# Kernel optimization log

Hardware: AMD Instinct MI355X
Metric: run time of the kernel (lower is better)

The kernel has to match this reference:

```python
import jax, jax.numpy as jnp
import numpy as np

EMBED_DIM = 512
NUM_HEADS = 8
HEAD_DIM = EMBED_DIM // NUM_HEADS
SCALE = 1.0 / HEAD_DIM ** 0.5


def setup_inputs() -> dict:
    key = jax.random.key(0)
    ks = jax.random.split(key, 7)
    B, C, H, W = 8, EMBED_DIM, 32, 32
    x = jax.random.normal(ks[0], (B, C, H, W), dtype=jnp.float32)
    s = 1.0 / np.sqrt(EMBED_DIM)
    return {
        "x": x,
        "ln_gamma": jnp.ones((EMBED_DIM,), jnp.float32),
        "ln_beta": jnp.zeros((EMBED_DIM,), jnp.float32),
        "w_qkv": jax.random.uniform(ks[1], (EMBED_DIM, 3 * EMBED_DIM), jnp.float32, -s, s),
        "b_qkv": jax.random.uniform(ks[2], (3 * EMBED_DIM,), jnp.float32, -s, s),
        "w_proj": jax.random.uniform(ks[3], (EMBED_DIM, EMBED_DIM), jnp.float32, -s, s),
        "b_proj": jax.random.uniform(ks[4], (EMBED_DIM,), jnp.float32, -s, s),
    }


def reference(x, ln_gamma, ln_beta, w_qkv, b_qkv, w_proj, b_proj):
    B, C, H, W = x.shape
    N = H * W
    # LayerNorm over channel dim (applied in NHWC layout in the original)
    xs = x.reshape(B, C, N).transpose(0, 2, 1)  # [B, N, C]
    mu = jnp.mean(xs, axis=-1, keepdims=True)
    var = jnp.mean(jnp.square(xs - mu), axis=-1, keepdims=True)
    xn = (xs - mu) / jnp.sqrt(var + 1e-5) * ln_gamma + ln_beta
    # QKV projection
    qkv = xn @ w_qkv + b_qkv                        # [B, N, 3C]
    qkv = qkv.reshape(B, N, 3, NUM_HEADS, HEAD_DIM)
    q = qkv[:, :, 0].transpose(0, 2, 1, 3)         # [B, h, N, d]
    k = qkv[:, :, 1].transpose(0, 2, 1, 3)
    v = qkv[:, :, 2].transpose(0, 2, 1, 3)
    # Scaled dot-product attention (full N x N scores, as in source)
    attn = jnp.einsum('bhnd,bhmd->bhnm', q, k) * SCALE
    attn = jax.nn.softmax(attn, axis=-1)
    o = jnp.einsum('bhnm,bhmd->bhnd', attn, v)     # [B, h, N, d]
    o = o.transpose(0, 2, 1, 3).reshape(B, N, C)
    # Output projection (dropout is identity in eval)
    o = o @ w_proj + b_proj
    return o.transpose(0, 2, 1).reshape(B, C, H, W)
```

## Files before the change

kernel.cpp:

```cpp
#include <hip/hip_runtime.h>
#include <hip/hip_bf16.h>
#include <math.h>

#define B_   8
#define C_   512
#define NH_  8
#define HD_  64
#define NSP  1024
#define M_   (B_*NSP)
#define NQKV 1536
#define SCALE_ 0.125f
#define S2L_  0.18033688f

typedef __attribute__((ext_vector_type(8))) __bf16 bf16x8;
typedef __attribute__((ext_vector_type(4))) float  f32x4;

__device__ __forceinline__ unsigned short f2bf(float f) {
  unsigned int u = __float_as_uint(f);
  u = u + 0x7fffu + ((u >> 16) & 1u);
  return (unsigned short)(u >> 16);
}

__device__ __forceinline__ unsigned int pk2bf(float a, float b) {
  __hip_bfloat162 t = __float22bfloat162_rn(make_float2(a, b));
  unsigned int u; __builtin_memcpy(&u, &t, 4);
  return u;
}

__device__ __forceinline__ void async16(const unsigned short* g, unsigned short* l) {
  __builtin_amdgcn_global_load_lds(
      (const __attribute__((address_space(1))) void*)g,
      (__attribute__((address_space(3))) void*)l, 16, 0, 0);
}

__global__ void ln_stats_kernel(const float* __restrict__ x,
                                float* __restrict__ psum,
                                float* __restrict__ psum2) {
  int tx = threadIdx.x & 31, ty = threadIdx.x >> 5;
  int cg  = blockIdx.x & 3;
  int nch = (blockIdx.x >> 2) & 31;
  int b   = blockIdx.x >> 7;
  int n0 = nch * 32;
  const float* xp = x + (size_t)b * C_ * NSP + n0 + tx;
  float s = 0.f, s2 = 0.f;
  for (int c = cg * 128 + ty; c < cg * 128 + 128; c += 8) {
    float v = xp[(size_t)c * NSP];
    s += v; s2 += v * v;
  }
  __shared__ float sh_s[8][32], sh_s2[8][32];
  sh_s[ty][tx] = s; sh_s2[ty][tx] = s2;
  __syncthreads();
  if (ty == 0) {
    float S = 0.f, S2 = 0.f;
    for (int j = 0; j < 8; j++) { S += sh_s[j][tx]; S2 += sh_s2[j][tx]; }
    psum [cg * M_ + b * NSP + n0 + tx] = S;
    psum2[cg * M_ + b * NSP + n0 + tx] = S2;
  }
}

__global__ __launch_bounds__(256) void applyw_kernel(
    const float* __restrict__ x, const float* __restrict__ psum,
    const float* __restrict__ psum2, const float* __restrict__ gamma,
    const float* __restrict__ beta, const float* __restrict__ wqkv,
    const float* __restrict__ wproj, unsigned short* __restrict__ xn,
    unsigned short* __restrict__ wqkvT, unsigned short* __restrict__ wprojT) {
  int tid = threadIdx.x;
  __shared__ float tile[64][65];
  int tx = tid & 63, ty = tid >> 6;
  if (blockIdx.x >= 1024) {
    const float* W; unsigned short* WT; int NW, t;
    if (blockIdx.x < 1216) { W = wqkv;  WT = wqkvT;  NW = NQKV; t = blockIdx.x - 1024; }
    else                   { W = wproj; WT = wprojT; NW = C_;   t = blockIdx.x - 1216; }
    int ntiles = NW >> 6;
    int kt = t / ntiles, nt = t - kt * ntiles;
    for (int i = ty; i < 64; i += 4)
      tile[i][tx] = W[(size_t)(kt * 64 + i) * NW + nt * 64 + tx];
    __syncthreads();
    for (int i = ty; i < 64; i += 4)
      WT[(size_t)(nt * 64 + i) * C_ + kt * 64 + tx] = f2bf(tile[tx][i]);
    return;
  }
  __shared__ float smu[64], srs[64];
  int c0 = (blockIdx.x & 7) * 64;
  int n0 = ((blockIdx.x >> 3) & 15) * 64;
  int b  = blockIdx.x >> 7;
  if (tid < 64) {
    int n = b * NSP + n0 + tid;
    float s  = psum [n] + psum [M_ + n] + psum [2 * M_ + n] + psum [3 * M_ + n];
    float s2 = psum2[n] + psum2[M_ + n] + psum2[2 * M_ + n] + psum2[3 * M_ + n];
    float mu = s * (1.0f / C_);
    float var = s2 * (1.0f / C_) - mu * mu;
    smu[tid] = mu;
    srs[tid] = rsqrtf(var + 1e-5f);
  }
  const float* xp = x + ((size_t)b * C_ + c0) * NSP + n0;
  for (int i = ty; i < 64; i += 4)
    tile[i][tx] = xp[(size_t)i * NSP + tx];
  __syncthreads();
  float g = gamma[c0 + tx], be = beta[c0 + tx];
  unsigned short* op = xn + ((size_t)(b * NSP + n0)) * C_ + c0 + tx;
  for (int i = ty; i < 64; i += 4) {
    float v = (tile[tx][i] - smu[i]) * srs[i] * g + be;
    op[(size_t)i * C_] = f2bf(v);
  }
}

__global__ __launch_bounds__(256) void gemm_qkv_kernel(
    const unsigned short* __restrict__ A,
    const unsigned short* __restrict__ Bt,
    const float* __restrict__ bias,
    unsigned short* __restrict__ out0, unsigned short* __restrict__ out1) {
  __shared__ __align__(16) char smem[24576];
  int tid = threadIdx.x;
  int wave = tid >> 6, lane = tid & 63, quad = lane >> 4, l15 = lane & 15;
  int n0 = blockIdx.x * 128, m0 = blockIdx.y * 64;
  int wm = (wave >> 1) * 32, wn = (wave & 1) * 64;
  int srow = lane >> 2, schunk = (lane & 3) * 8;
  auto stage = [&](int k0, int buf) {
    unsigned short* As = (unsigned short*)(smem + buf * 12288);
    unsigned short* Bs = (unsigned short*)(smem + buf * 12288 + 4096);
    async16(A + (size_t)(m0 + wave * 16 + srow) * 512 + k0 + schunk,
            As + wave * 16 * 32 + lane * 8);
#pragma unroll
    for (int j = 0; j < 2; j++) {
      int r0 = (wave + 4 * j) * 16;
      async16(Bt + (size_t)(n0 + r0 + srow) * 512 + k0 + schunk, Bs + r0 * 32 + lane * 8);
    }
  };
  f32x4 acc[2][4] = {};
  stage(0, 0);
  for (int kt = 0; kt < 16; kt++) {
    int cur = kt & 1;
    __syncthreads();
    if (kt < 15) stage((kt + 1) * 32, cur ^ 1);
    unsigned short* As = (unsigned short*)(smem + cur * 12288);
    unsigned short* Bs = (unsigned short*)(smem + cur * 12288 + 4096);
    bf16x8 a[2], bb[4];
#pragma unroll
    for (int mt = 0; mt < 2; mt++)
      a[mt] = *(const bf16x8*)(As + (wm + mt * 16 + l15) * 32 + quad * 8);
#pragma unroll
    for (int nt = 0; nt < 4; nt++)
      bb[nt] = *(const bf16x8*)(Bs + (wn + nt * 16 + l15) * 32 + quad * 8);
#pragma unroll
    for (int mt = 0; mt < 2; mt++)
#pragma unroll
      for (int nt = 0; nt < 4; nt++)
        acc[mt][nt] = __builtin_amdgcn_mfma_f32_16x16x32_bf16(
            a[mt], bb[nt], acc[mt][nt], 0, 0, 0);
  }
  if (n0 < 1024) {
    float sc = ((n0 + wn) < 512) ? S2L_ : 1.0f;
#pragma unroll
    for (int mt = 0; mt < 2; mt++)
#pragma unroll
      for (int nt = 0; nt < 4; nt++)
#pragma unroll
        for (int r = 0; r < 4; r++) {
          int row = m0 + wm + mt * 16 + quad * 4 + r;
          int col = n0 + wn + nt * 16 + l15;
          out0[(size_t)row * 1024 + col] = f2bf((acc[mt][nt][r] + bias[col]) * sc);
        }
  } else {
    __syncthreads();
    unsigned short* buf = (unsigned short*)smem + wave * (32 * 17);
    int b = m0 >> 10, nbase = m0 & 1023;
    for (int nc = 0; nc < 4; nc++) {
#pragma unroll
      for (int mt = 0; mt < 2; mt++)
#pragma unroll
        for (int r = 0; r < 4; r++) {
          int col = n0 + wn + nc * 16 + l15;
          buf[(mt * 16 + quad * 4 + r) * 17 + l15] = f2bf(acc[mt][nc][r] + bias[col]);
        }
      int ml = lane & 31;
#pragma unroll
      for (int j = 0; j < 8; j++) {
        int cl = j * 2 + (lane >> 5);
        int crel = n0 - 1024 + wn + nc * 16 + cl;
        out1[((size_t)b * C_ + crel) * NSP + nbase + wm + ml] = buf[ml * 17 + cl];
      }
    }
  }
}

__global__ __launch_bounds__(256) void gemm_proj_kernel(
    const unsigned short* __restrict__ A,
    const unsigned short* __restrict__ Bt,
    const float* __restrict__ bias,
    float* __restrict__ O) {
  __shared__ __align__(16) char smem[20480];
  int tid = threadIdx.x;
  int wave = tid >> 6, lane = tid & 63, quad = lane >> 4, l15 = lane & 15;
  int n0 = blockIdx.x * 128, m0 = blockIdx.y * 32;
  int wm = (wave >> 1) * 16, wn = (wave & 1) * 64;
  int srow = lane >> 2, schunk = (lane & 3) * 8;
  auto stage = [&](int k0, int buf) {
    unsigned short* As = (unsigned short*)(smem + buf * 10240);
    unsigned short* Bs = (unsigned short*)(smem + buf * 10240 + 2048);
    if (wave < 2)
      async16(A + (size_t)(m0 + wave * 16 + srow) * 512 + k0 + schunk,
              As + wave * 16 * 32 + lane * 8);
#pragma unroll
    for (int j = 0; j < 2; j++) {
      int r0 = (wave + 4 * j) * 16;
      async16(Bt + (size_t)(n0 + r0 + srow) * 512 + k0 + schunk, Bs + r0 * 32 + lane * 8);
    }
  };
  f32x4 acc[4] = {};
  stage(0, 0);
  for (int kt = 0; kt < 16; kt++) {
    int cur = kt & 1;
    __syncthreads();
    if (kt < 15) stage((kt + 1) * 32, cur ^ 1);
    unsigned short* As = (unsigned short*)(smem + cur * 10240);
    unsigned short* Bs = (unsigned short*)(smem + cur * 10240 + 2048);
    bf16x8 a, bb[4];
    a = *(const bf16x8*)(As + (wm + l15) * 32 + quad * 8);
#pragma unroll
    for (int nt = 0; nt < 4; nt++)
      bb[nt] = *(const bf16x8*)(Bs + (wn + nt * 16 + l15) * 32 + quad * 8);
#pragma unroll
    for (int nt = 0; nt < 4; nt++)
      acc[nt] = __builtin_amdgcn_mfma_f32_16x16x32_bf16(a, bb[nt], acc[nt], 0, 0, 0);
  }
  __syncthreads();
  float* buf = (float*)smem + wave * (16 * 17);
  int b = m0 >> 10, nbase = m0 & 1023;
  int ml = lane & 15, cg = lane >> 4;
  for (int nc = 0; nc < 4; nc++) {
#pragma unroll
    for (int r = 0; r < 4; r++) {
      int col = n0 + wn + nc * 16 + l15;
      buf[(quad * 4 + r) * 17 + l15] = acc[nc][r] + bias[col];
    }
#pragma unroll
    for (int j = 0; j < 4; j++) {
      int cl = j * 4 + cg;
      int c = n0 + wn + nc * 16 + cl;
      O[((size_t)b * C_ + c) * NSP + nbase + wm + ml] = buf[ml * 17 + cl];
    }
  }
}

__global__ __launch_bounds__(256, 3) void attn_kernel(
    const unsigned short* __restrict__ qk,
    const unsigned short* __restrict__ vt,
    unsigned short* __restrict__ o_ws) {
  __shared__ __align__(16) unsigned short Ks[2][2][32][64];
  __shared__ __align__(16) unsigned short Vts[2][2][64][32];
  __shared__ __align__(16) unsigned short Ps[4][32][36];
  __shared__ __align__(16) float Cb[2][16][68];
  __shared__ float Lb[2][16];
  int tid = threadIdx.x;
  int wave = tid >> 6, lane = tid & 63, quad = lane >> 4, l15 = lane & 15;
  int qw = wave & 1, kh = wave >> 1;
  int b = blockIdx.x >> 3, h = blockIdx.x & 7;
  int q0 = blockIdx.y * 64 + qw * 32;
  int srow = lane >> 3, scc = lane & 7, swzK = scc ^ srow;
  int srow4 = lane >> 2, scc4 = lane & 3, swzV = scc4 ^ ((srow4 >> 1) & 3);
  uint4 ones4 = (l15 == 0) ? make_uint4(0x3F803F80u, 0x3F803F80u, 0x3F803F80u, 0x3F803F80u)
                           : make_uint4(0u, 0u, 0u, 0u);
  bf16x8 av5; __builtin_memcpy(&av5, &ones4, 16);
  bf16x8 bq[2][2];
#pragma unroll
  for (int mt = 0; mt < 2; mt++)
#pragma unroll
    for (int ks = 0; ks < 2; ks++)
      bq[mt][ks] = *(const bf16x8*)(
          qk + (size_t)(b * NSP + q0 + mt * 16 + l15) * 1024 +
          h * 64 + ks * 32 + quad * 8);
  auto stage = [&](int it, int buf) {
    int k0 = kh * 512 + it * 32;
#pragma unroll
    for (int g = 0; g < 2; g++) {
      int krow = qw * 16 + g * 8;
      async16(qk + (size_t)(b * NSP + k0 + krow + srow) * 1024 + 512 + h * 64 + swzK * 8,
              &Ks[buf][kh][krow][0]);
      int vrow = qw * 32 + g * 16;
      async16(vt + ((size_t)(b * C_ + h * 64 + vrow + srow4)) * NSP + k0 + swzV * 8,
              &Vts[buf][kh][vrow][0]);
    }
  };
  f32x4 ot[4][2] = {};
  f32x4 lacc[2] = {};
  stage(0, 0);
  for (int it = 0; it < 16; it++) {
    int cur = it & 1;
    __syncthreads();
    if (it < 15) stage(it + 1, cur ^ 1);
    bf16x8 ak[2][2];
#pragma unroll
    for (int n4 = 0; n4 < 2; n4++)
#pragma unroll
      for (int ks = 0; ks < 2; ks++)
        ak[n4][ks] = *(const bf16x8*)(
            &Ks[cur][kh][n4 * 16 + l15][((ks * 4 + quad) ^ (l15 & 7)) * 8]);
    f32x4 s[2][2] = {};
#pragma unroll
    for (int n4 = 0; n4 < 2; n4++)
#pragma unroll
      for (int mt = 0; mt < 2; mt++)
#pragma unroll
        for (int ks = 0; ks < 2; ks++)
          s[n4][mt] = __builtin_amdgcn_mfma_f32_16x16x32_bf16(
              ak[n4][ks], bq[mt][ks], s[n4][mt], 0, 0, 0);
#pragma unroll
    for (int mt = 0; mt < 2; mt++)
#pragma unroll
      for (int n4 = 0; n4 < 2; n4++) {
        float p0 = __builtin_amdgcn_exp2f(s[n4][mt][0]);
        float p1 = __builtin_amdgcn_exp2f(s[n4][mt][1]);
        float p2 = __builtin_amdgcn_exp2f(s[n4][mt][2]);
        float p3 = __builtin_amdgcn_exp2f(s[n4][mt][3]);
        *(uint2*)(&Ps[wave][mt * 16 + l15][n4 * 16 + quad * 4]) =
            make_uint2(pk2bf(p0, p1), pk2bf(p2, p3));
      }
    bf16x8 av[4], bp[2];
#pragma unroll
    for (int dt = 0; dt < 4; dt++)
      av[dt] = *(const bf16x8*)(
          &Vts[cur][kh][dt * 16 + l15][(quad ^ ((l15 >> 1) & 3)) * 8]);
#pragma unroll
    for (int mt = 0; mt < 2; mt++)
      bp[mt] = *(const bf16x8*)(&Ps[wave][mt * 16 + l15][quad * 8]);
#pragma unroll
    for (int dt = 0; dt < 4; dt++)
#pragma unroll
      for (int mt = 0; mt < 2; mt++)
        ot[dt][mt] = __builtin_amdgcn_mfma_f32_16x16x32_bf16(
            av[dt], bp[mt], ot[dt][mt], 0, 0, 0);
#pragma unroll
    for (int mt = 0; mt < 2; mt++)
      lacc[mt] = __builtin_amdgcn_mfma_f32_16x16x32_bf16(
          av5, bp[mt], lacc[mt], 0, 0, 0);
  }
#pragma unroll
  for (int mt = 0; mt < 2; mt++) {
    __syncthreads();
    if (kh == 1) {
#pragma unroll
      for (int dt = 0; dt < 4; dt++)
        *(f32x4*)&Cb[qw][l15][dt * 16 + quad * 4] = ot[dt][mt];
      if (quad == 0) Lb[qw][l15] = lacc[mt][0];
    }
    __syncthreads();
    if (kh == 0) {
#pragma unroll
      for (int dt = 0; dt < 4; dt++)
        ot[dt][mt] += *(const f32x4*)&Cb[qw][l15][dt * 16 + quad * 4];
      float lsum = lacc[mt][0] + Lb[qw][l15];
      float lv = __shfl(lsum, l15);
      float inv = 1.f / lv;
      size_t rowoff = (size_t)(b * NSP + q0 + mt * 16 + l15) * 512 + h * 64;
#pragma unroll
      for (int dt = 0; dt < 4; dt++)
        *(uint2*)(o_ws + rowoff + dt * 16 + quad * 4) =
            make_uint2(pk2bf(ot[dt][mt][0] * inv, ot[dt][mt][1] * inv),
                       pk2bf(ot[dt][mt][2] * inv, ot[dt][mt][3] * inv));
    }
  }
}

extern "C" void kernel_launch(void* const* d_in, const int* in_sizes, int n_in,
                              void* d_out, int out_size, void* d_ws, size_t ws_size,
                              hipStream_t stream) {
  const float* x     = (const float*)d_in[0];
  const float* gamma = (const float*)d_in[1];
  const float* beta  = (const float*)d_in[2];
  const float* wqkv  = (const float*)d_in[3];
  const float* bqkv  = (const float*)d_in[4];
  const float* wproj = (const float*)d_in[5];
  const float* bproj = (const float*)d_in[6];
  char* ws = (char*)d_ws;
  float*          psum   = (float*)ws;
  float*          psum2  = (float*)(ws + 131072);
  unsigned short* wqkvT  = (unsigned short*)(ws + 262144);
  unsigned short* wprojT = (unsigned short*)(ws + 1835008);
  unsigned short* qk_bf  = (unsigned short*)(ws + 2359296);
  unsigned short* vt_bf  = (unsigned short*)(ws + 19136512);
  unsigned short* xn_bf  = (unsigned short*)(ws + 27525120);
  unsigned short* o_bf   = xn_bf;
  float* out = (float*)d_out;

  ln_stats_kernel<<<1024, 256, 0, stream>>>(x, psum, psum2);
  applyw_kernel<<<1024 + 192 + 64, 256, 0, stream>>>(x, psum, psum2, gamma, beta,
                                                     wqkv, wproj, xn_bf, wqkvT, wprojT);
  gemm_qkv_kernel<<<dim3(NQKV / 128, M_ / 64), 256, 0, stream>>>(
      xn_bf, wqkvT, bqkv, qk_bf, vt_bf);
  attn_kernel<<<dim3(B_ * NH_, NSP / 64), 256, 0, stream>>>(qk_bf, vt_bf, o_bf);
  gemm_proj_kernel<<<dim3(C_ / 128, M_ / 32), 256, 0, stream>>>(
      o_bf, wprojT, bproj, out);
}
```

Measured before the change: 162.7 us.

## Rewrite attention with 32x32x16 MFMA, register-resident P and no split-K reduction

The attention kernel now uses 32x32x16 bf16 MFMAs, with each wave owning 32 query rows across the full key range. This removes the two-way key split and its LDS reduction. The probabilities are repacked in registers using v_permlane32_swap instead of going through an LDS P buffer, and the row sum is accumulated with scalar adds instead of an extra MFMA against a ones vector. Each block covers 128 queries with 64-key tiles, which halves the grid and lowers the occupancy target to 2 blocks, trading parallelism for fewer LDS round trips and less sync.

```diff
diff --git a/kernel.cpp b/kernel.cpp
--- a/kernel.cpp
+++ b/kernel.cpp
@@ -14,6 +14,7 @@
 
 typedef __attribute__((ext_vector_type(8))) __bf16 bf16x8;
 typedef __attribute__((ext_vector_type(4))) float  f32x4;
+typedef __attribute__((ext_vector_type(16))) float f32x16;
 
 __device__ __forceinline__ unsigned short f2bf(float f) {
   unsigned int u = __float_as_uint(f);
@@ -243,122 +244,97 @@
   }
 }
 
-__global__ __launch_bounds__(256, 3) void attn_kernel(
+__global__ __launch_bounds__(256, 2) void attn_kernel(
     const unsigned short* __restrict__ qk,
     const unsigned short* __restrict__ vt,
     unsigned short* __restrict__ o_ws) {
-  __shared__ __align__(16) unsigned short Ks[2][2][32][64];
-  __shared__ __align__(16) unsigned short Vts[2][2][64][32];
-  __shared__ __align__(16) unsigned short Ps[4][32][36];
-  __shared__ __align__(16) float Cb[2][16][68];
-  __shared__ float Lb[2][16];
+  __shared__ __align__(16) unsigned short Ks[2][64][64];
+  __shared__ __align__(16) unsigned short Vts[2][64][64];
   int tid = threadIdx.x;
-  int wave = tid >> 6, lane = tid & 63, quad = lane >> 4, l15 = lane & 15;
-  int qw = wave & 1, kh = wave >> 1;
+  int wave = tid >> 6, lane = tid & 63;
+  int l31 = lane & 31, hi = lane >> 5;
   int b = blockIdx.x >> 3, h = blockIdx.x & 7;
-  int q0 = blockIdx.y * 64 + qw * 32;
-  int srow = lane >> 3, scc = lane & 7, swzK = scc ^ srow;
-  int srow4 = lane >> 2, scc4 = lane & 3, swzV = scc4 ^ ((srow4 >> 1) & 3);
-  uint4 ones4 = (l15 == 0) ? make_uint4(0x3F803F80u, 0x3F803F80u, 0x3F803F80u, 0x3F803F80u)
-                           : make_uint4(0u, 0u, 0u, 0u);
-  bf16x8 av5; __builtin_memcpy(&av5, &ones4, 16);
-  bf16x8 bq[2][2];
-#pragma unroll
-  for (int mt = 0; mt < 2; mt++)
-#pragma unroll
-    for (int ks = 0; ks < 2; ks++)
-      bq[mt][ks] = *(const bf16x8*)(
-          qk + (size_t)(b * NSP + q0 + mt * 16 + l15) * 1024 +
-          h * 64 + ks * 32 + quad * 8);
+  int qb = blockIdx.y * 128 + wave * 32;
+  int sc8 = lane & 7, sr8 = lane >> 3;
+  int swz = sc8 ^ sr8;
+  bf16x8 bq[4];
+#pragma unroll
+  for (int ks = 0; ks < 4; ks++)
+    bq[ks] = *(const bf16x8*)(
+        qk + (size_t)(b * NSP + qb + l31) * 1024 + h * 64 + ks * 16 + hi * 8);
   auto stage = [&](int it, int buf) {
-    int k0 = kh * 512 + it * 32;
+    int k0 = it * 64;
 #pragma unroll
     for (int g = 0; g < 2; g++) {
-      int krow = qw * 16 + g * 8;
-      async16(qk + (size_t)(b * NSP + k0 + krow + srow) * 1024 + 512 + h * 64 + swzK * 8,
-              &Ks[buf][kh][krow][0]);
-      int vrow = qw * 32 + g * 16;
-      async16(vt + ((size_t)(b * C_ + h * 64 + vrow + srow4)) * NSP + k0 + swzV * 8,
-              &Vts[buf][kh][vrow][0]);
+      int row = wave * 16 + g * 8 + sr8;
+      async16(qk + (size_t)(b * NSP + k0 + row) * 1024 + 512 + h * 64 + swz * 8,
+              &Ks[buf][wave * 16 + g * 8][0]);
+      async16(vt + ((size_t)(b * C_ + h * 64 + row)) * NSP + k0 + swz * 8,
+              &Vts[buf][wave * 16 + g * 8][0]);
     }
   };
-  f32x4 ot[4][2] = {};
-  f32x4 lacc[2] = {};
+  f32x16 ot0 = {}, ot1 = {};
+  float lsum = 0.f;
   stage(0, 0);
   for (int it = 0; it < 16; it++) {
     int cur = it & 1;
     __syncthreads();
     if (it < 15) stage(it + 1, cur ^ 1);
-    bf16x8 ak[2][2];
-#pragma unroll
-    for (int n4 = 0; n4 < 2; n4++)
-#pragma unroll
-      for (int ks = 0; ks < 2; ks++)
-        ak[n4][ks] = *(const bf16x8*)(
-            &Ks[cur][kh][n4 * 16 + l15][((ks * 4 + quad) ^ (l15 & 7)) * 8]);
-    f32x4 s[2][2] = {};
-#pragma unroll
-    for (int n4 = 0; n4 < 2; n4++)
-#pragma unroll
-      for (int mt = 0; mt < 2; mt++)
-#pragma unroll
-        for (int ks = 0; ks < 2; ks++)
-          s[n4][mt] = __builtin_amdgcn_mfma_f32_16x16x32_bf16(
-              ak[n4][ks], bq[mt][ks], s[n4][mt], 0, 0, 0);
-#pragma unroll
-    for (int mt = 0; mt < 2; mt++)
-#pragma unroll
-      for (int n4 = 0; n4 < 2; n4++) {
-        float p0 = __builtin_amdgcn_exp2f(s[n4][mt][0]);
-        float p1 = __builtin_amdgcn_exp2f(s[n4][mt][1]);
-        float p2 = __builtin_amdgcn_exp2f(s[n4][mt][2]);
-        float p3 = __builtin_amdgcn_exp2f(s[n4][mt][3]);
-        *(uint2*)(&Ps[wave][mt * 16 + l15][n4 * 16 + quad * 4]) =
-            make_uint2(pk2bf(p0, p1), pk2bf(p2, p3));
+    bf16x8 bp[4];
+#pragma unroll
+    for (int kt = 0; kt < 2; kt++) {
+      f32x16 s = {};
+#pragma unroll
+      for (int ks = 0; ks < 4; ks++) {
+        bf16x8 ak = *(const bf16x8*)(
+            &Ks[cur][kt * 32 + l31][((ks * 2 + hi) ^ (l31 & 7)) * 8]);
+        s = __builtin_amdgcn_mfma_f32_32x32x16_bf16(ak, bq[ks], s, 0, 0, 0);
       }
-    bf16x8 av[4], bp[2];
-#pragma unroll
-    for (int dt = 0; dt < 4; dt++)
-      av[dt] = *(const bf16x8*)(
-          &Vts[cur][kh][dt * 16 + l15][(quad ^ ((l15 >> 1) & 3)) * 8]);
-#pragma unroll
-    for (int mt = 0; mt < 2; mt++)
-      bp[mt] = *(const bf16x8*)(&Ps[wave][mt * 16 + l15][quad * 8]);
-#pragma unroll
-    for (int dt = 0; dt < 4; dt++)
-#pragma unroll
-      for (int mt = 0; mt < 2; mt++)
-        ot[dt][mt] = __builtin_amdgcn_mfma_f32_16x16x32_bf16(
-            av[dt], bp[mt], ot[dt][mt], 0, 0, 0);
-#pragma unroll
-    for (int mt = 0; mt < 2; mt++)
-      lacc[mt] = __builtin_amdgcn_mfma_f32_16x16x32_bf16(
-          av5, bp[mt], lacc[mt], 0, 0, 0);
-  }
-#pragma unroll
-  for (int mt = 0; mt < 2; mt++) {
-    __syncthreads();
-    if (kh == 1) {
-#pragma unroll
-      for (int dt = 0; dt < 4; dt++)
-        *(f32x4*)&Cb[qw][l15][dt * 16 + quad * 4] = ot[dt][mt];
-      if (quad == 0) Lb[qw][l15] = lacc[mt][0];
-    }
-    __syncthreads();
-    if (kh == 0) {
-#pragma unroll
-      for (int dt = 0; dt < 4; dt++)
-        ot[dt][mt] += *(const f32x4*)&Cb[qw][l15][dt * 16 + quad * 4];
-      float lsum = lacc[mt][0] + Lb[qw][l15];
-      float lv = __shfl(lsum, l15);
-      float inv = 1.f / lv;
-      size_t rowoff = (size_t)(b * NSP + q0 + mt * 16 + l15) * 512 + h * 64;
-#pragma unroll
-      for (int dt = 0; dt < 4; dt++)
-        *(uint2*)(o_ws + rowoff + dt * 16 + quad * 4) =
-            make_uint2(pk2bf(ot[dt][mt][0] * inv, ot[dt][mt][1] * inv),
-                       pk2bf(ot[dt][mt][2] * inv, ot[dt][mt][3] * inv));
-    }
+      float p0 = __builtin_amdgcn_exp2f(s[0]),  p1 = __builtin_amdgcn_exp2f(s[1]);
+      float p2 = __builtin_amdgcn_exp2f(s[2]),  p3 = __builtin_amdgcn_exp2f(s[3]);
+      float p4 = __builtin_amdgcn_exp2f(s[4]),  p5 = __builtin_amdgcn_exp2f(s[5]);
+      float p6 = __builtin_amdgcn_exp2f(s[6]),  p7 = __builtin_amdgcn_exp2f(s[7]);
+      float p8 = __builtin_amdgcn_exp2f(s[8]),  p9 = __builtin_amdgcn_exp2f(s[9]);
+      float pa = __builtin_amdgcn_exp2f(s[10]), pb = __builtin_amdgcn_exp2f(s[11]);
+      float pc = __builtin_amdgcn_exp2f(s[12]), pd = __builtin_amdgcn_exp2f(s[13]);
+      float pe = __builtin_amdgcn_exp2f(s[14]), pf = __builtin_amdgcn_exp2f(s[15]);
+      lsum += ((p0 + p1) + (p2 + p3)) + ((p4 + p5) + (p6 + p7)) +
+              (((p8 + p9) + (pa + pb)) + ((pc + pd) + (pe + pf)));
+      unsigned int d0 = pk2bf(p0, p1), d1 = pk2bf(p2, p3);
+      unsigned int d2 = pk2bf(p4, p5), d3 = pk2bf(p6, p7);
+      unsigned int d4 = pk2bf(p8, p9), d5 = pk2bf(pa, pb);
+      unsigned int d6 = pk2bf(pc, pd), d7 = pk2bf(pe, pf);
+      asm volatile("v_permlane32_swap_b32 %0, %1" : "+v"(d0), "+v"(d2));
+      asm volatile("v_permlane32_swap_b32 %0, %1" : "+v"(d1), "+v"(d3));
+      asm volatile("v_permlane32_swap_b32 %0, %1" : "+v"(d4), "+v"(d6));
+      asm volatile("v_permlane32_swap_b32 %0, %1" : "+v"(d5), "+v"(d7));
+      uint4 f0 = make_uint4(d0, d1, d2, d3);
+      uint4 f1 = make_uint4(d4, d5, d6, d7);
+      __builtin_memcpy(&bp[kt * 2 + 0], &f0, 16);
+      __builtin_memcpy(&bp[kt * 2 + 1], &f1, 16);
+    }
+#pragma unroll
+    for (int kc = 0; kc < 4; kc++) {
+      bf16x8 av0 = *(const bf16x8*)(
+          &Vts[cur][l31][((kc * 2 + hi) ^ (l31 & 7)) * 8]);
+      ot0 = __builtin_amdgcn_mfma_f32_32x32x16_bf16(av0, bp[kc], ot0, 0, 0, 0);
+      bf16x8 av1 = *(const bf16x8*)(
+          &Vts[cur][32 + l31][(((kc * 2 + hi) ^ (l31 & 7)) ^ 0) * 8]);
+      ot1 = __builtin_amdgcn_mfma_f32_32x32x16_bf16(av1, bp[kc], ot1, 0, 0, 0);
+    }
+  }
+  float lv = __shfl(lsum, l31) + __shfl(lsum, l31 + 32);
+  float inv = 1.f / lv;
+  unsigned short* orow = o_ws + (size_t)(b * NSP + qb + l31) * 512 + h * 64;
+#pragma unroll
+  for (int g = 0; g < 4; g++) {
+    int d0 = 8 * g + 4 * hi;
+    *(uint2*)(orow + d0) =
+        make_uint2(pk2bf(ot0[4 * g + 0] * inv, ot0[4 * g + 1] * inv),
+                   pk2bf(ot0[4 * g + 2] * inv, ot0[4 * g + 3] * inv));
+    *(uint2*)(orow + 32 + d0) =
+        make_uint2(pk2bf(ot1[4 * g + 0] * inv, ot1[4 * g + 1] * inv),
+                   pk2bf(ot1[4 * g + 2] * inv, ot1[4 * g + 3] * inv));
   }
 }
 
@@ -388,7 +364,7 @@
                                                      wqkv, wproj, xn_bf, wqkvT, wprojT);
   gemm_qkv_kernel<<<dim3(NQKV / 128, M_ / 64), 256, 0, stream>>>(
       xn_bf, wqkvT, bqkv, qk_bf, vt_bf);
-  attn_kernel<<<dim3(B_ * NH_, NSP / 64), 256, 0, stream>>>(qk_bf, vt_bf, o_bf);
+  attn_kernel<<<dim3(B_ * NH_, NSP / 64 / 2), 256, 0, stream>>>(qk_bf, vt_bf, o_bf);
   gemm_proj_kernel<<<dim3(C_ / 128, M_ / 32), 256, 0, stream>>>(
       o_bf, wprojT, bproj, out);
 }
```

Result: faster. 155.6 us (-4.4%).
